# Optimization experiments

Hardware: AMD Instinct MI355X
Metric: run time of the kernel (lower is better)

Reference implementation:

```python
import jax, jax.numpy as jnp
import numpy as np

B, S, E, H = 2, 2048, 1024, 16
HD = E // H  # 64
NEG = -1e24


def setup_inputs() -> dict:
    key = jax.random.key(0)
    ks = jax.random.split(key, 20)
    sc_e = 1.0 / np.sqrt(E)
    inp = {
        "q_matrix": jax.random.normal(ks[0], (B, S, E), jnp.float32),
        "k_matrix": jax.random.normal(ks[1], (B, S, E), jnp.float32),
        "v_matrix": jax.random.normal(ks[2], (B, S, E), jnp.float32),
        "mask": jax.random.randint(ks[3], (B, S, S), 0, 2).astype(bool),
        # global QKV projections (embed_dim -> embed_dim)
        "Wq": jax.random.normal(ks[4], (E, E), jnp.float32) * sc_e,
        "bq": jnp.zeros((E,), jnp.float32),
        "Wk": jax.random.normal(ks[5], (E, E), jnp.float32) * sc_e,
        "bk": jnp.zeros((E,), jnp.float32),
        "Wv": jax.random.normal(ks[6], (E, E), jnp.float32) * sc_e,
        "bv": jnp.zeros((E,), jnp.float32),
        # per-head QKV projections (embed_dim -> head_dim), batched over heads
        "Whq": jax.random.normal(ks[7], (H, E, HD), jnp.float32) * sc_e,
        "bhq": jnp.zeros((H, HD), jnp.float32),
        "Whk": jax.random.normal(ks[8], (H, E, HD), jnp.float32) * sc_e,
        "bhk": jnp.zeros((H, HD), jnp.float32),
        "Whv": jax.random.normal(ks[9], (H, E, HD), jnp.float32) * sc_e,
        "bhv": jnp.zeros((H, HD), jnp.float32),
        # output projection
        "Wo": jax.random.normal(ks[10], (E, E), jnp.float32) * sc_e,
        "bo": jnp.zeros((E,), jnp.float32),
    }
    return inp


def reference(q_matrix, k_matrix, v_matrix, mask, Wq, bq, Wk, bk, Wv, bv,
              Whq, bhq, Whk, bhk, Whv, bhv, Wo, bo):
    # global projections [B,S,E]
    qg = q_matrix @ Wq + bq
    kg = k_matrix @ Wk + bk
    vg = v_matrix @ Wv + bv
    # per-head projections -> [B,H,S,HD]
    qh = jnp.einsum('bse,hed->bhsd', qg, Whq) + bhq[None, :, None, :]
    kh = jnp.einsum('bse,hed->bhsd', kg, Whk) + bhk[None, :, None, :]
    vh = jnp.einsum('bse,hed->bhsd', vg, Whv) + bhv[None, :, None, :]
    # scaled dot-product attention, scores [B,H,S,S]
    scores = jnp.einsum('bhsd,bhtd->bhst', qh, kh) / jnp.sqrt(jnp.float32(HD))
    scores = jnp.where(mask[:, None, :, :], NEG, scores)
    weights = jax.nn.softmax(scores, axis=-1)
    out = jnp.einsum('bhst,bhtd->bhsd', weights, vh)
    # concat heads (head order along last dim, matching torch.cat)
    x = out.transpose(0, 2, 1, 3).reshape(out.shape[0], out.shape[2], E)
    return x @ Wo + bo
```

## Files before the change

### kernel.cpp

```cpp
#include <hip/hip_runtime.h>
#include <hip/hip_bf16.h>

typedef unsigned short us16;
typedef __attribute__((ext_vector_type(8))) short short8;
typedef __attribute__((ext_vector_type(4))) float float4v;

#define E_DIM 1024
#define S_LEN 2048
#define B_DIM 2
#define H_DIM 16
#define HD_DIM 64
#define M_ROWS 4096

__device__ __forceinline__ float b2f(us16 b) {
    return __uint_as_float(((unsigned int)b) << 16);
}
__device__ __forceinline__ us16 f2b(float f) {
    unsigned int u = __float_as_uint(f);
    unsigned int r = (u + 0x7fffu + ((u >> 16) & 1u)) >> 16;
    return (us16)r;
}
__device__ __forceinline__ us16 f2b_fast(float f) {
    return (us16)((__float_as_uint(f) + 0x8000u) >> 16);
}

__device__ __forceinline__ void gload16(const us16* g, us16* lds_uniform_base) {
    __builtin_amdgcn_global_load_lds(
        (const __attribute__((address_space(1))) void*)g,
        (__attribute__((address_space(3))) void*)lds_uniform_base, 16, 0, 0);
}

__global__ __launch_bounds__(256) void prep(
    const float* __restrict__ q, const float* __restrict__ k, const float* __restrict__ v,
    const float* __restrict__ Wq, const float* __restrict__ Wk, const float* __restrict__ Wv,
    const float* __restrict__ Whq, const float* __restrict__ Whk, const float* __restrict__ Whv,
    const float* __restrict__ Wo,
    const float* __restrict__ bq, const float* __restrict__ bk, const float* __restrict__ bv,
    const float* __restrict__ bhq, const float* __restrict__ bhk, const float* __restrict__ bhv,
    const int* __restrict__ mask,
    us16* qb, us16* kb, us16* vb, us16* Wqb, us16* Wkb, us16* Wvb,
    us16* WhqT, us16* WhkT, us16* WhvT, us16* WoT,
    unsigned long long* mbits,
    float* bcq, float* bck, float* bcv, float* zbias)
{
    __shared__ us16 tile[32][33];
    __shared__ float red[4][64];
    int blk = blockIdx.x, tid = threadIdx.x;

    if (blk < 7680) {
        const float* in; us16* out; int idx;
        if (blk < 6144) {
            int z = blk >> 11, rem = blk & 2047;
            in = z == 0 ? q : z == 1 ? k : v;
            out = z == 0 ? qb : z == 1 ? kb : vb;
            idx = (rem * 256 + tid) * 8;
        } else {
            int t = blk - 6144, z = t >> 9, rem = t & 511;
            in = z == 0 ? Wq : z == 1 ? Wk : Wv;
            out = z == 0 ? Wqb : z == 1 ? Wkb : Wvb;
            idx = (rem * 256 + tid) * 8;
        }
        float4 f0 = *(const float4*)(in + idx);
        float4 f1 = *(const float4*)(in + idx + 4);
        us16 t8[8] = {f2b(f0.x), f2b(f0.y), f2b(f0.z), f2b(f0.w),
                      f2b(f1.x), f2b(f1.y), f2b(f1.z), f2b(f1.w)};
        *(uint4*)(out + idx) = *(const uint4*)t8;
    } else if (blk < 11776) {
        int t = blk - 7680, z = t >> 10, rem = t & 1023;
        const float* in = z == 0 ? Whq : z == 1 ? Whk : z == 2 ? Whv : Wo;
        us16* out = z == 0 ? WhqT : z == 1 ? WhkT : z == 2 ? WhvT : WoT;
        int mode = (z < 3) ? 1 : 0;
        int bx = rem & 31, by = rem >> 5;
        int tx = tid & 31, ty = tid >> 5;
#pragma unroll
        for (int i = 0; i < 4; ++i) {
            int e = by * 32 + ty + i * 8;
            int c = bx * 32 + tx;
            size_t src;
            if (mode == 0) src = (size_t)e * E_DIM + c;
            else           src = ((size_t)(c >> 6) * E_DIM + e) * 64 + (c & 63);
            tile[ty + i * 8][tx] = f2b(in[src]);
        }
        __syncthreads();
#pragma unroll
        for (int i = 0; i < 4; ++i) {
            int c = bx * 32 + ty + i * 8;
            int e = by * 32 + tx;
            out[(size_t)c * E_DIM + e] = tile[tx][ty + i * 8];
        }
    } else if (blk < 12800) {
        int row = (blk - 11776) * 4 + (tid >> 6);
        int lane = tid & 63;
        const int* mp = mask + (size_t)row * S_LEN;
        for (int w = 0; w < 32; ++w) {
            int mv = mp[w * 64 + lane];
            unsigned long long bal = __ballot(mv != 0);
            if (lane == 0) mbits[(size_t)row * 32 + w] = bal;
        }
    } else if (blk < 12848) {
        int t = blk - 12800, z = t >> 4, h = t & 15;
        const float* bg = z == 0 ? bq : z == 1 ? bk : bv;
        const float* Wh = z == 0 ? Whq : z == 1 ? Whk : Whv;
        const float* bh = z == 0 ? bhq : z == 1 ? bhk : bhv;
        float* bc = z == 0 ? bcq : z == 1 ? bck : bcv;
        int d = tid & 63, part = tid >> 6;
        float acc = 0.f;
        int j0 = part * 256;
        for (int j = j0; j < j0 + 256; ++j)
            acc += bg[j] * Wh[((size_t)h * E_DIM + j) * HD_DIM + d];
        red[part][d] = acc;
        __syncthreads();
        if (tid < 64)
            bc[h * 64 + tid] = red[0][tid] + red[1][tid] + red[2][tid] + red[3][tid] + bh[h * 64 + tid];
    } else {
        int i = (blk - 12848) * 256 + tid;
        if (i < 1024) zbias[i] = 0.f;
    }
}

#define BK 32

__device__ __forceinline__ void gemm_body(
    const us16* __restrict__ A, const us16* __restrict__ Bt,
    const float* __restrict__ bias, void* __restrict__ Cp,
    int M, int N, int K, int bxt, int byt, int omode)
{
    __shared__ us16 As[128 * BK];
    __shared__ us16 Bs[128 * BK];

    int tid = threadIdx.x;
    int wave = tid >> 6, lane = tid & 63;
    int quad = lane >> 4, l16 = lane & 15;
    int wm = (wave >> 1) * 64, wn = (wave & 1) * 64;
    int bm0 = byt * 128, bn0 = bxt * 128;
    int srow = lane >> 2;
    int gcol = (((lane & 3) ^ (srow & 3)) << 3);
    int rslot = ((quad ^ (l16 & 3)) << 3);

    float4v acc[4][4];
#pragma unroll
    for (int i = 0; i < 4; ++i)
#pragma unroll
        for (int j = 0; j < 4; ++j)
#pragma unroll
            for (int r = 0; r < 4; ++r) acc[i][j][r] = 0.f;

    for (int k0 = 0; k0 < K; k0 += BK) {
#pragma unroll
        for (int c = 0; c < 2; ++c) {
            int r0 = 32 * wave + 16 * c;
            gload16(A  + (size_t)(bm0 + r0 + srow) * K + k0 + gcol, &As[r0 * BK]);
            gload16(Bt + (size_t)(bn0 + r0 + srow) * K + k0 + gcol, &Bs[r0 * BK]);
        }
        __syncthreads();
        short8 af[4], bfr[4];
#pragma unroll
        for (int i = 0; i < 4; ++i)
            af[i] = *(const short8*)&As[(wm + i * 16 + l16) * BK + rslot];
#pragma unroll
        for (int j = 0; j < 4; ++j)
            bfr[j] = *(const short8*)&Bs[(wn + j * 16 + l16) * BK + rslot];
#pragma unroll
        for (int i = 0; i < 4; ++i)
#pragma unroll
            for (int j = 0; j < 4; ++j)
                acc[i][j] = __builtin_amdgcn_mfma_f32_16x16x32_bf16(af[i], bfr[j], acc[i][j], 0, 0, 0);
        __syncthreads();
    }

#pragma unroll
    for (int i = 0; i < 4; ++i) {
#pragma unroll
        for (int j = 0; j < 4; ++j) {
#pragma unroll
            for (int r = 0; r < 4; ++r) {
                int row = bm0 + wm + i * 16 + quad * 4 + r;
                int col = bn0 + wn + j * 16 + l16;
                float vv = acc[i][j][r] + ((omode == 3) ? bias[row] : bias[col]);
                if (omode == 1) {
                    int b = row >> 11, s = row & 2047, h = col >> 6, d = col & 63;
                    ((us16*)Cp)[(((size_t)(b * H_DIM + h) * S_LEN + s) * HD_DIM) + d] = f2b(vv);
                } else {
                    int h = row >> 6, d = row & 63, b = col >> 11, sl = col & 2047;
                    ((us16*)Cp)[(((size_t)(b * H_DIM + h) * HD_DIM + d) * S_LEN) + sl] = f2b(vv);
                }
            }
        }
    }
}

__global__ __launch_bounds__(256) void proj_all(
    const us16* __restrict__ qb, const us16* __restrict__ kb, const us16* __restrict__ vb,
    const us16* __restrict__ WcqT, const us16* __restrict__ WckT, const us16* __restrict__ WcvT,
    const float* __restrict__ bcq, const float* __restrict__ bck, const float* __restrict__ bcv,
    us16* __restrict__ qhb, us16* __restrict__ khb, us16* __restrict__ vtb)
{
    int bx = blockIdx.x;
    int z = bx >> 8, t = bx & 255;
    if (z == 0)      gemm_body(qb, WcqT, bcq, qhb, M_ROWS, E_DIM, E_DIM, t & 7, t >> 3, 1);
    else if (z == 1) gemm_body(kb, WckT, bck, khb, M_ROWS, E_DIM, E_DIM, t & 7, t >> 3, 1);
    else             gemm_body(WcvT, vb, bcv, vtb, E_DIM, M_ROWS, E_DIM, t & 31, t >> 5, 3);
}

template<int OMODE>
__device__ __forceinline__ void gemm64_body(
    const us16* __restrict__ A, const us16* __restrict__ Bt,
    const float* __restrict__ bias, void* __restrict__ Cp,
    int M, int N, int K, int bxt, int byt)
{
    __shared__ us16 As[64 * BK];
    __shared__ us16 Bs[128 * BK];

    int tid = threadIdx.x;
    int wave = tid >> 6, lane = tid & 63;
    int quad = lane >> 4, l16 = lane & 15;
    int wm = (wave >> 1) * 32, wn = (wave & 1) * 64;
    int bm0 = byt * 64, bn0 = bxt * 128;
    int srow = lane >> 2;
    int gcol = (((lane & 3) ^ (srow & 3)) << 3);
    int rslot = ((quad ^ (l16 & 3)) << 3);

    float4v acc[2][4];
#pragma unroll
    for (int i = 0; i < 2; ++i)
#pragma unroll
        for (int j = 0; j < 4; ++j)
#pragma unroll
            for (int r = 0; r < 4; ++r) acc[i][j][r] = 0.f;

    for (int k0 = 0; k0 < K; k0 += BK) {
        gload16(A + (size_t)(bm0 + 16 * wave + srow) * K + k0 + gcol, &As[16 * wave * BK]);
#pragma unroll
        for (int c = 0; c < 2; ++c) {
            int r0 = 32 * wave + 16 * c;
            gload16(Bt + (size_t)(bn0 + r0 + srow) * K + k0 + gcol, &Bs[r0 * BK]);
        }
        __syncthreads();
        short8 af[2], bfr[4];
#pragma unroll
        for (int i = 0; i < 2; ++i)
            af[i] = *(const short8*)&As[(wm + i * 16 + l16) * BK + rslot];
#pragma unroll
        for (int j = 0; j < 4; ++j)
            bfr[j] = *(const short8*)&Bs[(wn + j * 16 + l16) * BK + rslot];
#pragma unroll
        for (int i = 0; i < 2; ++i)
#pragma unroll
            for (int j = 0; j < 4; ++j)
                acc[i][j] = __builtin_amdgcn_mfma_f32_16x16x32_bf16(af[i], bfr[j], acc[i][j], 0, 0, 0);
        __syncthreads();
    }

#pragma unroll
    for (int i = 0; i < 2; ++i)
#pragma unroll
        for (int j = 0; j < 4; ++j)
#pragma unroll
            for (int r = 0; r < 4; ++r) {
                int row = bm0 + wm + i * 16 + quad * 4 + r;
                int col = bn0 + wn + j * 16 + l16;
                float vv = acc[i][j][r] + bias[col];
                if (OMODE == 0) ((us16*)Cp)[(size_t)row * N + col] = f2b(vv);
                else            ((float*)Cp)[(size_t)row * N + col] = vv;
            }
}

__global__ __launch_bounds__(256) void wgemm3(
    const us16* A0, const us16* A1, const us16* A2,
    const us16* B0, const us16* B1, const us16* B2,
    const float* zbias, us16* C0, us16* C1, us16* C2)
{
    int z = blockIdx.z;
    const us16* A = z == 0 ? A0 : z == 1 ? A1 : A2;
    const us16* Bt = z == 0 ? B0 : z == 1 ? B1 : B2;
    us16* C = z == 0 ? C0 : z == 1 ? C1 : C2;
    gemm64_body<0>(A, Bt, zbias, C, E_DIM, E_DIM, E_DIM, blockIdx.x, blockIdx.y);
}

__global__ __launch_bounds__(256) void gemm_out64(
    const us16* __restrict__ A, const us16* __restrict__ Bt,
    const float* __restrict__ bias, float* __restrict__ C, int M, int N, int K)
{
    gemm64_body<2>(A, Bt, bias, C, M, N, K, blockIdx.x, blockIdx.y);
}

#define LDK 72
#define LDP 76
#define SCALE2 0.18033688011112042f

__global__ __launch_bounds__(512) void attn_kernel(
    const us16* __restrict__ qh, const us16* __restrict__ kh,
    const us16* __restrict__ vt, const unsigned long long* __restrict__ mbits,
    us16* __restrict__ o_p, float* __restrict__ l_p)
{
    __shared__ us16 Ks[64 * LDK];
    __shared__ us16 Vs[64 * LDK];
    __shared__ us16 Pw[8][16 * LDP];

    int tid = threadIdx.x;
    int w = tid >> 6, lane = tid & 63;
    int quad = lane >> 4, l16 = lane & 15;
    int bh = blockIdx.y;
    int b = bh >> 4;
    int z = blockIdx.z;
    int q0 = blockIdx.x * 128;
    const size_t base = (size_t)bh * (S_LEN * HD_DIM);

    short8 qf0, qf1;
    {
        int qrow = q0 + w * 16 + l16;
        const us16* qp = qh + base + (size_t)qrow * HD_DIM + quad * 8;
        qf0 = *(const short8*)qp;
        qf1 = *(const short8*)(qp + 32);
    }

    float l_i[4];
    float4v o[4];
#pragma unroll
    for (int r = 0; r < 4; ++r) l_i[r] = 0.f;
#pragma unroll
    for (int dt = 0; dt < 4; ++dt)
#pragma unroll
        for (int r = 0; r < 4; ++r) o[dt][r] = 0.f;

    int qb = q0 + w * 16 + quad * 4;
    const unsigned long long* mrow = mbits + (size_t)(b * S_LEN + qb) * 32;

    int kend = z * 1024 + 1024;
    for (int kt = z * 1024; kt < kend; kt += 64) {
        __syncthreads();
        {
            int r = tid >> 3, cc = (tid & 7) * 8;
            *(uint4*)&Ks[r * LDK + cc] = *(const uint4*)(kh + base + (size_t)(kt + r) * HD_DIM + cc);
            *(uint4*)&Vs[r * LDK + cc] = *(const uint4*)(vt + base + (size_t)r * S_LEN + kt + cc);
        }
        __syncthreads();

        int kw = kt >> 6;
        unsigned long long mw[4];
#pragma unroll
        for (int r = 0; r < 4; ++r) mw[r] = mrow[r * 32 + kw];

        float4v sc[4];
#pragma unroll
        for (int ct = 0; ct < 4; ++ct) {
            short8 kf0 = *(const short8*)&Ks[(ct * 16 + l16) * LDK + quad * 8];
            short8 kf1 = *(const short8*)&Ks[(ct * 16 + l16) * LDK + 32 + quad * 8];
            float4v a;
#pragma unroll
            for (int r = 0; r < 4; ++r) a[r] = 0.f;
            a = __builtin_amdgcn_mfma_f32_16x16x32_bf16(qf0, kf0, a, 0, 0, 0);
            a = __builtin_amdgcn_mfma_f32_16x16x32_bf16(qf1, kf1, a, 0, 0, 0);
            sc[ct] = a;
        }

#pragma unroll
        for (int ct = 0; ct < 4; ++ct) {
            int sh = ct * 16 + l16;
#pragma unroll
            for (int r = 0; r < 4; ++r) {
                float pin = ((mw[r] >> sh) & 1ull) ? -1e38f : sc[ct][r] * SCALE2;
                float p = __builtin_amdgcn_exp2f(pin);
                l_i[r] += p;
                Pw[w][(quad * 4 + r) * LDP + ct * 16 + l16] = f2b_fast(p);
            }
        }

        short8 pf0 = *(const short8*)&Pw[w][l16 * LDP + quad * 8];
        short8 pf1 = *(const short8*)&Pw[w][l16 * LDP + 32 + quad * 8];
#pragma unroll
        for (int dt = 0; dt < 4; ++dt) {
            short8 vf0 = *(const short8*)&Vs[(dt * 16 + l16) * LDK + quad * 8];
            short8 vf1 = *(const short8*)&Vs[(dt * 16 + l16) * LDK + 32 + quad * 8];
            o[dt] = __builtin_amdgcn_mfma_f32_16x16x32_bf16(pf0, vf0, o[dt], 0, 0, 0);
            o[dt] = __builtin_amdgcn_mfma_f32_16x16x32_bf16(pf1, vf1, o[dt], 0, 0, 0);
        }
    }

#pragma unroll
    for (int r = 0; r < 4; ++r) {
        float s = l_i[r];
        s += __shfl_xor(s, 1, 64);
        s += __shfl_xor(s, 2, 64);
        s += __shfl_xor(s, 4, 64);
        s += __shfl_xor(s, 8, 64);
        l_i[r] = s;
    }
    int rowg = bh * S_LEN + qb;
    if (l16 == 0) {
#pragma unroll
        for (int r = 0; r < 4; ++r) l_p[(size_t)z * 65536 + rowg + r] = l_i[r];
    }
#pragma unroll
    for (int dt = 0; dt < 4; ++dt)
#pragma unroll
        for (int r = 0; r < 4; ++r)
            o_p[(size_t)z * 4194304 + (size_t)(rowg + r) * 64 + dt * 16 + l16] = f2b(o[dt][r]);
}

__global__ __launch_bounds__(256) void attn_combine(
    const us16* __restrict__ o_p, const float* __restrict__ l_p,
    us16* __restrict__ x)
{
    int fidx = blockIdx.x * 256 + threadIdx.x;
    int rix = fidx >> 3;
    int d8 = (fidx & 7) * 8;
    float linv = 1.0f / (l_p[rix] + l_p[65536 + rix]);
    uint4 a = *(const uint4*)(o_p + (size_t)rix * 64 + d8);
    uint4 c = *(const uint4*)(o_p + 4194304 + (size_t)rix * 64 + d8);
    const us16* ap = (const us16*)&a;
    const us16* cp = (const us16*)&c;
    us16 t8[8];
#pragma unroll
    for (int i = 0; i < 8; ++i)
        t8[i] = f2b((b2f(ap[i]) + b2f(cp[i])) * linv);
    int bh = rix >> 11, b = bh >> 4, h = bh & 15, s = rix & 2047;
    *(uint4*)&x[(size_t)(b * S_LEN + s) * E_DIM + h * HD_DIM + d8] = *(const uint4*)t8;
}

extern "C" void kernel_launch(void* const* d_in, const int* in_sizes, int n_in,
                              void* d_out, int out_size, void* d_ws, size_t ws_size,
                              hipStream_t stream) {
    const float* q    = (const float*)d_in[0];
    const float* k    = (const float*)d_in[1];
    const float* v    = (const float*)d_in[2];
    const int*   mask = (const int*)d_in[3];
    const float* Wq = (const float*)d_in[4];   const float* bq = (const float*)d_in[5];
    const float* Wk = (const float*)d_in[6];   const float* bk = (const float*)d_in[7];
    const float* Wv = (const float*)d_in[8];   const float* bv = (const float*)d_in[9];
    const float* Whq = (const float*)d_in[10]; const float* bhq = (const float*)d_in[11];
    const float* Whk = (const float*)d_in[12]; const float* bhk = (const float*)d_in[13];
    const float* Whv = (const float*)d_in[14]; const float* bhv = (const float*)d_in[15];
    const float* Wo = (const float*)d_in[16];  const float* bo = (const float*)d_in[17];

    us16* ws = (us16*)d_ws;
    const size_t M1 = (size_t)1 << 20;
    us16* WhqT = ws + 0 * M1;
    us16* WhkT = ws + 1 * M1;
    us16* WhvT = ws + 2 * M1;
    us16* WoT  = ws + 3 * M1;
    us16* WcqT = ws + 4 * M1;
    us16* WckT = ws + 5 * M1;
    us16* WcvT = ws + 6 * M1;
    us16* Wqb  = ws + 7 * M1;
    us16* Wkb  = ws + 8 * M1;
    us16* Wvb  = ws + 9 * M1;
    us16* qb   = ws + 10 * M1;
    us16* kb   = ws + 14 * M1;
    us16* vb   = ws + 18 * M1;
    us16* qhb  = ws + 22 * M1;
    us16* khb  = ws + 26 * M1;
    us16* vtb  = ws + 30 * M1;
    us16* o_p  = qb;
    us16* xb   = vb;
    float* bcq   = (float*)(ws + 34 * M1);
    float* bck   = bcq + 1024;
    float* bcv   = bck + 1024;
    float* zbias = bcv + 1024;
    unsigned long long* mbits = (unsigned long long*)(ws + 34 * M1 + 16384);
    float* l_p = (float*)(ws + 34 * M1 + 16384 + 524288);

    prep<<<12852, 256, 0, stream>>>(q, k, v, Wq, Wk, Wv, Whq, Whk, Whv, Wo,
                                    bq, bk, bv, bhq, bhk, bhv, mask,
                                    qb, kb, vb, Wqb, Wkb, Wvb,
                                    WhqT, WhkT, WhvT, WoT, mbits,
                                    bcq, bck, bcv, zbias);

    wgemm3<<<dim3(8, 16, 3), 256, 0, stream>>>(WhqT, WhkT, WhvT, Wqb, Wkb, Wvb, zbias,
                                               WcqT, WckT, WcvT);

    proj_all<<<768, 256, 0, stream>>>(qb, kb, vb, WcqT, WckT, WcvT,
                                      bcq, bck, bcv, qhb, khb, vtb);

    attn_kernel<<<dim3(16, 32, 2), 512, 0, stream>>>(qhb, khb, vtb, mbits, o_p, l_p);
    attn_combine<<<2048, 256, 0, stream>>>(o_p, l_p, xb);

    gemm_out64<<<dim3(8, 64), 256, 0, stream>>>(xb, WoT, bo, (float*)d_out,
                                                M_ROWS, E_DIM, E_DIM);
}
```

Measured before the change: 339.4 us.

## Transpose score MFMA, swizzle K/V LDS via direct loads, fold scale into Q

Computes the score tile transposed (K as the A operand) so each lane owns one query row. The mask then becomes a single 64-bit word per tile and the row sum needs only two shuffles. P is written as packed bf16 pairs with 8-byte stores. K/V tiles are loaded straight into XOR-swizzled, unpadded LDS with global_load_lds, and the softmax scale is folded into the Q projection weights and bias to drop a multiply per score. Swizzled indexing and async-load ordering add correctness risk.

```diff
diff --git a/kernel.cpp b/kernel.cpp
--- a/kernel.cpp
+++ b/kernel.cpp
@@ -11,6 +11,7 @@
 #define H_DIM 16
 #define HD_DIM 64
 #define M_ROWS 4096
+#define SCALE2 0.18033688011112042f
 
 __device__ __forceinline__ float b2f(us16 b) {
     return __uint_as_float(((unsigned int)b) << 16);
@@ -20,8 +21,9 @@
     unsigned int r = (u + 0x7fffu + ((u >> 16) & 1u)) >> 16;
     return (us16)r;
 }
-__device__ __forceinline__ us16 f2b_fast(float f) {
-    return (us16)((__float_as_uint(f) + 0x8000u) >> 16);
+__device__ __forceinline__ unsigned pack2(float a, float b) {
+    return ((__float_as_uint(a) + 0x8000u) >> 16) |
+           ((__float_as_uint(b) + 0x8000u) & 0xFFFF0000u);
 }
 
 __device__ __forceinline__ void gload16(const us16* g, us16* lds_uniform_base) {
@@ -103,6 +105,7 @@
         const float* Wh = z == 0 ? Whq : z == 1 ? Whk : Whv;
         const float* bh = z == 0 ? bhq : z == 1 ? bhk : bhv;
         float* bc = z == 0 ? bcq : z == 1 ? bck : bcv;
+        float sc = (z == 0) ? SCALE2 : 1.0f;
         int d = tid & 63, part = tid >> 6;
         float acc = 0.f;
         int j0 = part * 256;
@@ -111,7 +114,7 @@
         red[part][d] = acc;
         __syncthreads();
         if (tid < 64)
-            bc[h * 64 + tid] = red[0][tid] + red[1][tid] + red[2][tid] + red[3][tid] + bh[h * 64 + tid];
+            bc[h * 64 + tid] = (red[0][tid] + red[1][tid] + red[2][tid] + red[3][tid] + bh[h * 64 + tid]) * sc;
     } else {
         int i = (blk - 12848) * 256 + tid;
         if (i < 1024) zbias[i] = 0.f;
@@ -206,7 +209,7 @@
 __device__ __forceinline__ void gemm64_body(
     const us16* __restrict__ A, const us16* __restrict__ Bt,
     const float* __restrict__ bias, void* __restrict__ Cp,
-    int M, int N, int K, int bxt, int byt)
+    int M, int N, int K, int bxt, int byt, float oscale)
 {
     __shared__ us16 As[64 * BK];
     __shared__ us16 Bs[128 * BK];
@@ -259,7 +262,7 @@
             for (int r = 0; r < 4; ++r) {
                 int row = bm0 + wm + i * 16 + quad * 4 + r;
                 int col = bn0 + wn + j * 16 + l16;
-                float vv = acc[i][j][r] + bias[col];
+                float vv = (acc[i][j][r] + bias[col]) * oscale;
                 if (OMODE == 0) ((us16*)Cp)[(size_t)row * N + col] = f2b(vv);
                 else            ((float*)Cp)[(size_t)row * N + col] = vv;
             }
@@ -274,28 +277,27 @@
     const us16* A = z == 0 ? A0 : z == 1 ? A1 : A2;
     const us16* Bt = z == 0 ? B0 : z == 1 ? B1 : B2;
     us16* C = z == 0 ? C0 : z == 1 ? C1 : C2;
-    gemm64_body<0>(A, Bt, zbias, C, E_DIM, E_DIM, E_DIM, blockIdx.x, blockIdx.y);
+    float sc = (z == 0) ? SCALE2 : 1.0f;
+    gemm64_body<0>(A, Bt, zbias, C, E_DIM, E_DIM, E_DIM, blockIdx.x, blockIdx.y, sc);
 }
 
 __global__ __launch_bounds__(256) void gemm_out64(
     const us16* __restrict__ A, const us16* __restrict__ Bt,
     const float* __restrict__ bias, float* __restrict__ C, int M, int N, int K)
 {
-    gemm64_body<2>(A, Bt, bias, C, M, N, K, blockIdx.x, blockIdx.y);
-}
-
-#define LDK 72
-#define LDP 76
-#define SCALE2 0.18033688011112042f
+    gemm64_body<2>(A, Bt, bias, C, M, N, K, blockIdx.x, blockIdx.y, 1.0f);
+}
+
+#define PST 72
 
 __global__ __launch_bounds__(512) void attn_kernel(
     const us16* __restrict__ qh, const us16* __restrict__ kh,
     const us16* __restrict__ vt, const unsigned long long* __restrict__ mbits,
     us16* __restrict__ o_p, float* __restrict__ l_p)
 {
-    __shared__ us16 Ks[64 * LDK];
-    __shared__ us16 Vs[64 * LDK];
-    __shared__ us16 Pw[8][16 * LDP];
+    __shared__ us16 Ks[64 * 64];
+    __shared__ us16 Vs[64 * 64];
+    __shared__ us16 Pw[8][16 * PST];
 
     int tid = threadIdx.x;
     int w = tid >> 6, lane = tid & 63;
@@ -306,91 +308,89 @@
     int q0 = blockIdx.x * 128;
     const size_t base = (size_t)bh * (S_LEN * HD_DIM);
 
+    int qrow = q0 + w * 16 + l16;
     short8 qf0, qf1;
     {
-        int qrow = q0 + w * 16 + l16;
         const us16* qp = qh + base + (size_t)qrow * HD_DIM + quad * 8;
         qf0 = *(const short8*)qp;
         qf1 = *(const short8*)(qp + 32);
     }
 
-    float l_i[4];
+    int strow = w * 8 + (lane >> 3);
+    int scol = ((lane & 7) ^ (strow & 7)) * 8;
+    us16* kdst = &Ks[w * 512];
+    us16* vdst = &Vs[w * 512];
+    const us16* ksrc0 = kh + base + (size_t)strow * HD_DIM + scol;
+    const us16* vsrc0 = vt + base + (size_t)strow * S_LEN + scol;
+
+    int slotA = (quad ^ (l16 & 7)) * 8;
+    int slotB = ((quad ^ (l16 & 7)) ^ 4) * 8;
+
+    float lsum = 0.f;
     float4v o[4];
 #pragma unroll
-    for (int r = 0; r < 4; ++r) l_i[r] = 0.f;
-#pragma unroll
     for (int dt = 0; dt < 4; ++dt)
 #pragma unroll
         for (int r = 0; r < 4; ++r) o[dt][r] = 0.f;
 
-    int qb = q0 + w * 16 + quad * 4;
-    const unsigned long long* mrow = mbits + (size_t)(b * S_LEN + qb) * 32;
-
-    int kend = z * 1024 + 1024;
-    for (int kt = z * 1024; kt < kend; kt += 64) {
-        __syncthreads();
-        {
-            int r = tid >> 3, cc = (tid & 7) * 8;
-            *(uint4*)&Ks[r * LDK + cc] = *(const uint4*)(kh + base + (size_t)(kt + r) * HD_DIM + cc);
-            *(uint4*)&Vs[r * LDK + cc] = *(const uint4*)(vt + base + (size_t)r * S_LEN + kt + cc);
-        }
-        __syncthreads();
-
-        int kw = kt >> 6;
-        unsigned long long mw[4];
-#pragma unroll
-        for (int r = 0; r < 4; ++r) mw[r] = mrow[r * 32 + kw];
+    const unsigned long long* mrow = mbits + ((size_t)(b * S_LEN + qrow) * 32) + z * 16;
+
+    for (int kt = z * 1024; kt < z * 1024 + 1024; kt += 64) {
+        __syncthreads();
+        gload16(ksrc0 + (size_t)kt * HD_DIM, kdst);
+        gload16(vsrc0 + kt, vdst);
+        __syncthreads();
+
+        unsigned long long mw = *mrow++;
 
         float4v sc[4];
 #pragma unroll
         for (int ct = 0; ct < 4; ++ct) {
-            short8 kf0 = *(const short8*)&Ks[(ct * 16 + l16) * LDK + quad * 8];
-            short8 kf1 = *(const short8*)&Ks[(ct * 16 + l16) * LDK + 32 + quad * 8];
+            int t = ct * 16 + l16;
+            short8 kf0 = *(const short8*)&Ks[t * 64 + slotA];
+            short8 kf1 = *(const short8*)&Ks[t * 64 + slotB];
             float4v a;
 #pragma unroll
             for (int r = 0; r < 4; ++r) a[r] = 0.f;
-            a = __builtin_amdgcn_mfma_f32_16x16x32_bf16(qf0, kf0, a, 0, 0, 0);
-            a = __builtin_amdgcn_mfma_f32_16x16x32_bf16(qf1, kf1, a, 0, 0, 0);
+            a = __builtin_amdgcn_mfma_f32_16x16x32_bf16(kf0, qf0, a, 0, 0, 0);
+            a = __builtin_amdgcn_mfma_f32_16x16x32_bf16(kf1, qf1, a, 0, 0, 0);
             sc[ct] = a;
         }
 
 #pragma unroll
         for (int ct = 0; ct < 4; ++ct) {
-            int sh = ct * 16 + l16;
+            unsigned bits = (unsigned)(mw >> (ct * 16 + quad * 4));
+            float p[4];
 #pragma unroll
             for (int r = 0; r < 4; ++r) {
-                float pin = ((mw[r] >> sh) & 1ull) ? -1e38f : sc[ct][r] * SCALE2;
-                float p = __builtin_amdgcn_exp2f(pin);
-                l_i[r] += p;
-                Pw[w][(quad * 4 + r) * LDP + ct * 16 + l16] = f2b_fast(p);
+                float pin = ((bits >> r) & 1u) ? -1e38f : sc[ct][r];
+                p[r] = __builtin_amdgcn_exp2f(pin);
+                lsum += p[r];
             }
-        }
-
-        short8 pf0 = *(const short8*)&Pw[w][l16 * LDP + quad * 8];
-        short8 pf1 = *(const short8*)&Pw[w][l16 * LDP + 32 + quad * 8];
+            uint2 pk;
+            pk.x = pack2(p[0], p[1]);
+            pk.y = pack2(p[2], p[3]);
+            *(uint2*)&Pw[w][l16 * PST + ct * 16 + quad * 4] = pk;
+        }
+
+        short8 pf0 = *(const short8*)&Pw[w][l16 * PST + quad * 8];
+        short8 pf1 = *(const short8*)&Pw[w][l16 * PST + 32 + quad * 8];
 #pragma unroll
         for (int dt = 0; dt < 4; ++dt) {
-            short8 vf0 = *(const short8*)&Vs[(dt * 16 + l16) * LDK + quad * 8];
-            short8 vf1 = *(const short8*)&Vs[(dt * 16 + l16) * LDK + 32 + quad * 8];
+            int d = dt * 16 + l16;
+            short8 vf0 = *(const short8*)&Vs[d * 64 + slotA];
+            short8 vf1 = *(const short8*)&Vs[d * 64 + slotB];
             o[dt] = __builtin_amdgcn_mfma_f32_16x16x32_bf16(pf0, vf0, o[dt], 0, 0, 0);
             o[dt] = __builtin_amdgcn_mfma_f32_16x16x32_bf16(pf1, vf1, o[dt], 0, 0, 0);
         }
     }
 
-#pragma unroll
-    for (int r = 0; r < 4; ++r) {
-        float s = l_i[r];
-        s += __shfl_xor(s, 1, 64);
-        s += __shfl_xor(s, 2, 64);
-        s += __shfl_xor(s, 4, 64);
-        s += __shfl_xor(s, 8, 64);
-        l_i[r] = s;
-    }
-    int rowg = bh * S_LEN + qb;
-    if (l16 == 0) {
-#pragma unroll
-        for (int r = 0; r < 4; ++r) l_p[(size_t)z * 65536 + rowg + r] = l_i[r];
-    }
+    lsum += __shfl_xor(lsum, 16, 64);
+    lsum += __shfl_xor(lsum, 32, 64);
+    if (lane < 16)
+        l_p[(size_t)z * 65536 + bh * S_LEN + qrow] = lsum;
+
+    int rowg = bh * S_LEN + q0 + w * 16 + quad * 4;
 #pragma unroll
     for (int dt = 0; dt < 4; ++dt)
 #pragma unroll
```

After: 323.5 us. -4.7%, faster.
